# Kernel tuning notes

Measured on AMD Instinct MI355X. Metric: run time of the kernel, lower is better.

## Reference

```python
import jax, jax.numpy as jnp
import numpy as np

D_MODEL = 1024
N_HEADS = 16
D_K = D_MODEL // N_HEADS
B, S = 4, 2048
NEG = -1e9


def setup_inputs() -> dict:
    key = jax.random.key(0)
    ks = jax.random.split(key, 9)
    scale = 1.0 / np.sqrt(D_MODEL)
    x = jax.random.normal(ks[0], (B, S, D_MODEL), dtype=jnp.float32)
    mask = jnp.tril(jnp.ones((S, S), dtype=jnp.int32))  # causal lower-triangular
    Wq = jax.random.normal(ks[1], (D_MODEL, D_MODEL), dtype=jnp.float32) * scale
    Wk = jax.random.normal(ks[2], (D_MODEL, D_MODEL), dtype=jnp.float32) * scale
    Wv = jax.random.normal(ks[3], (D_MODEL, D_MODEL), dtype=jnp.float32) * scale
    Wo = jax.random.normal(ks[4], (D_MODEL, D_MODEL), dtype=jnp.float32) * scale
    bq = jnp.zeros((D_MODEL,), dtype=jnp.float32)
    bk = jnp.zeros((D_MODEL,), dtype=jnp.float32)
    bv = jnp.zeros((D_MODEL,), dtype=jnp.float32)
    bo = jnp.zeros((D_MODEL,), dtype=jnp.float32)
    return {"x": x, "mask": mask, "Wq": Wq, "bq": bq, "Wk": Wk, "bk": bk,
            "Wv": Wv, "bv": bv, "Wo": Wo, "bo": bo}


def reference(x, mask, Wq, bq, Wk, bk, Wv, bv, Wo, bo):
    b, s, _ = x.shape
    # nn.Linear: y = x @ W.T + b
    Q = x @ Wq.T + bq
    K = x @ Wk.T + bk
    V = x @ Wv.T + bv
    # [b, h, s, d_k]
    Q = Q.reshape(b, s, N_HEADS, D_K).transpose(0, 2, 1, 3)
    K = K.reshape(b, s, N_HEADS, D_K).transpose(0, 2, 1, 3)
    V = V.reshape(b, s, N_HEADS, D_K).transpose(0, 2, 1, 3)
    score = jnp.einsum('bhqd,bhkd->bhqk', Q, K) / jnp.sqrt(jnp.float32(D_K))
    score = jnp.where(mask == 0, jnp.float32(NEG), score)
    attn = jax.nn.softmax(score, axis=-1)
    out = jnp.einsum('bhqk,bhkd->bhqd', attn, V)
    out = out.transpose(0, 2, 1, 3).reshape(b, s, D_MODEL)
    return out @ Wo.T + bo
```

## Files before the change

### kernel.cpp

```cpp
#include <hip/hip_runtime.h>
#include <hip/hip_bf16.h>
#include <stdint.h>

typedef __bf16 bf16x8 __attribute__((ext_vector_type(8)));
typedef float  f32x4  __attribute__((ext_vector_type(4)));

#define B_   4
#define S_   2048
#define DM   1024
#define H_   16
#define DK   64
#define M_TOT 8192

__device__ __forceinline__ void gld16(const __bf16* g, char* l) {
    __builtin_amdgcn_global_load_lds(
        (const __attribute__((address_space(1))) void*)g,
        (__attribute__((address_space(3))) void*)l,
        16, 0, 0);
}

__global__ __launch_bounds__(256)
void cvt_f32_bf16(const float* __restrict__ in, __bf16* __restrict__ out, int n) {
    int i = (blockIdx.x * 256 + threadIdx.x) * 8;
    if (i >= n) return;
    float4 a = *(const float4*)(in + i);
    float4 c = *(const float4*)(in + i + 4);
    bf16x8 o;
    o[0] = (__bf16)a.x; o[1] = (__bf16)a.y; o[2] = (__bf16)a.z; o[3] = (__bf16)a.w;
    o[4] = (__bf16)c.x; o[5] = (__bf16)c.y; o[6] = (__bf16)c.z; o[7] = (__bf16)c.w;
    *(bf16x8*)(out + i) = o;
}

__global__ __launch_bounds__(256)
void cvt4_w(const float* __restrict__ w0, const float* __restrict__ w1,
            const float* __restrict__ w2, const float* __restrict__ w3,
            __bf16* __restrict__ out) {
    const int z = blockIdx.z;
    const float* in = (z == 0) ? w0 : (z == 1) ? w1 : (z == 2) ? w2 : w3;
    int i = (blockIdx.x * 256 + threadIdx.x) * 8;
    float4 a = *(const float4*)(in + i);
    float4 c = *(const float4*)(in + i + 4);
    bf16x8 o;
    o[0] = (__bf16)a.x; o[1] = (__bf16)a.y; o[2] = (__bf16)a.z; o[3] = (__bf16)a.w;
    o[4] = (__bf16)c.x; o[5] = (__bf16)c.y; o[6] = (__bf16)c.z; o[7] = (__bf16)c.w;
    *(bf16x8*)(out + (size_t)z * (DM * DM) + i) = o;
}

__device__ __forceinline__ void gemm_core(const __bf16* __restrict__ A,
                                          const __bf16* __restrict__ W,
                                          int m0, int n0,
                                          f32x4 (&acc)[4][4]) {
    __shared__ __bf16 As[128 * 32];
    __shared__ __bf16 Bs[128 * 32];
    const int tid  = threadIdx.x;
    const int wid  = tid >> 6;
    const int lane = tid & 63;
    const int ln15 = lane & 15, lg = lane >> 4;
    const int wr = (wid >> 1) * 64;
    const int wc = (wid & 1) * 64;

    const int c1 = tid, c2 = tid + 256;
    const int ar1 = m0 + (c1 >> 2), ac1 = (c1 & 3) * 8;
    const int ar2 = m0 + (c2 >> 2), ac2 = (c2 & 3) * 8;
    const int br1 = n0 + (c1 >> 2);
    const int br2 = n0 + (c2 >> 2);
    char* la1 = (char*)As + wid * 1024;
    char* la2 = la1 + 4096;
    char* lb1 = (char*)Bs + wid * 1024;
    char* lb2 = lb1 + 4096;

    for (int k0 = 0; k0 < DM; k0 += 32) {
        gld16(A + (size_t)ar1 * DM + k0 + ac1, la1);
        gld16(A + (size_t)ar2 * DM + k0 + ac2, la2);
        gld16(W + (size_t)br1 * DM + k0 + ac1, lb1);
        gld16(W + (size_t)br2 * DM + k0 + ac2, lb2);
        __syncthreads();
        bf16x8 af[4], bfr[4];
#pragma unroll
        for (int m = 0; m < 4; ++m)
            af[m] = *(const bf16x8*)&As[(wr + m * 16 + ln15) * 32 + lg * 8];
#pragma unroll
        for (int n = 0; n < 4; ++n)
            bfr[n] = *(const bf16x8*)&Bs[(wc + n * 16 + ln15) * 32 + lg * 8];
#pragma unroll
        for (int m = 0; m < 4; ++m)
#pragma unroll
            for (int n = 0; n < 4; ++n)
                acc[m][n] = __builtin_amdgcn_mfma_f32_16x16x32_bf16(af[m], bfr[n], acc[m][n], 0, 0, 0);
        __syncthreads();
    }
}

__global__ __launch_bounds__(256)
void gemm_qkv_kernel(const __bf16* __restrict__ Xb,
                     const __bf16* __restrict__ Wq, const __bf16* __restrict__ Wk,
                     const __bf16* __restrict__ Wv,
                     const float* __restrict__ bq, const float* __restrict__ bk,
                     const float* __restrict__ bv,
                     __bf16* __restrict__ Qb, __bf16* __restrict__ Kb,
                     __bf16* __restrict__ Vt) {
    const int z = blockIdx.z;
    const __bf16* W   = (z == 0) ? Wq : (z == 1) ? Wk : Wv;
    const float* bias = (z == 0) ? bq : (z == 1) ? bk : bv;
    const int m0 = blockIdx.x * 128, n0 = blockIdx.y * 128;

    f32x4 acc[4][4] = {};
    gemm_core(Xb, W, m0, n0, acc);

    const int tid = threadIdx.x, wid = tid >> 6, lane = tid & 63;
    const int ln15 = lane & 15, lg = lane >> 4;
    const int wr = (wid >> 1) * 64, wc = (wid & 1) * 64;
    const float oscl = (z == 0) ? 0.18033688f : 1.0f;

    if (z < 2) {
        __bf16* out = (z == 0) ? Qb : Kb;
#pragma unroll
        for (int ni = 0; ni < 4; ++ni) {
            int col = n0 + wc + ni * 16 + ln15;
            int h = col >> 6, d = col & 63;
            float bval = bias[col];
#pragma unroll
            for (int mi = 0; mi < 4; ++mi)
#pragma unroll
                for (int r = 0; r < 4; ++r) {
                    int row = m0 + wr + mi * 16 + lg * 4 + r;
                    int b = row >> 11, s = row & 2047;
                    out[(((size_t)(b * H_ + h)) * S_ + s) * DK + d] =
                        (__bf16)((acc[mi][ni][r] + bval) * oscl);
                }
        }
    } else {
#pragma unroll
        for (int ni = 0; ni < 4; ++ni) {
            int col = n0 + wc + ni * 16 + ln15;
            int h = col >> 6, d = col & 63;
            float bval = bias[col];
#pragma unroll
            for (int mi = 0; mi < 4; ++mi)
#pragma unroll
                for (int r = 0; r < 4; ++r) {
                    int row = m0 + wr + mi * 16 + lg * 4 + r;
                    int b = row >> 11, s = row & 2047;
                    Vt[(((size_t)(b * H_ + h)) * DK + d) * S_ + s] =
                        (__bf16)(acc[mi][ni][r] + bval);
                }
        }
    }
}

__global__ __launch_bounds__(256)
void gemm_out_kernel(const __bf16* __restrict__ Ab, const __bf16* __restrict__ Wo,
                     const float* __restrict__ bo, float* __restrict__ out) {
    const int m0 = blockIdx.x * 128, n0 = blockIdx.y * 128;
    f32x4 acc[4][4] = {};
    gemm_core(Ab, Wo, m0, n0, acc);

    const int tid = threadIdx.x, wid = tid >> 6, lane = tid & 63;
    const int ln15 = lane & 15, lg = lane >> 4;
    const int wr = (wid >> 1) * 64, wc = (wid & 1) * 64;
#pragma unroll
    for (int ni = 0; ni < 4; ++ni) {
        int col = n0 + wc + ni * 16 + ln15;
        float bval = bo[col];
#pragma unroll
        for (int mi = 0; mi < 4; ++mi)
#pragma unroll
            for (int r = 0; r < 4; ++r) {
                int row = m0 + wr + mi * 16 + lg * 4 + r;
                out[(size_t)row * DM + col] = acc[mi][ni][r] + bval;
            }
    }
}

__global__ __launch_bounds__(512)
void attn_kernel(const __bf16* __restrict__ Qb, const __bf16* __restrict__ Kb,
                 const __bf16* __restrict__ Vt, __bf16* __restrict__ AO) {
    __shared__ __bf16 Ks[2][64 * 64];
    __shared__ __bf16 Vs[2][64 * 64];

    const int tid = threadIdx.x, wid = tid >> 6, lane = tid & 63;
    const int ln15 = lane & 15, lg = lane >> 4;
    const int bh = blockIdx.y;
    const size_t base = (size_t)bh * (S_ * DK);
    const int b = bh >> 4, h = bh & 15;

    const int sr = tid >> 3;
    const int sc = ((tid & 7) ^ (sr & 7)) * 8;
    const int swz = (ln15 & 7) << 3;

    const __bf16* kgb = Kb + base;
    const __bf16* vgb = Vt + base;

    auto stage = [&](int buf, int kt) {
        char* dk = (char*)Ks + buf * 8192 + wid * 1024;
        char* dv = (char*)Vs + buf * 8192 + wid * 1024;
        gld16(kgb + (size_t)(kt * 64 + sr) * DK + sc, dk);
        gld16(vgb + (size_t)sr * S_ + kt * 64 + sc, dv);
    };

#pragma unroll
    for (int ph = 0; ph < 2; ++ph) {
        const int qb   = ph ? (int)blockIdx.x : 15 - (int)blockIdx.x;
        const int last = 2 * qb + 1;
        const int dt   = 2 * qb + (wid >> 2);
        const int qr0  = qb * 128 + wid * 16 + ln15;

        bf16x8 qf[2];
        {
            int q0 = qb * 128 + wid * 16 + ln15;
            qf[0] = *(const bf16x8*)&Qb[base + (size_t)q0 * DK + lg * 8];
            qf[1] = *(const bf16x8*)&Qb[base + (size_t)q0 * DK + 32 + lg * 8];
        }

        f32x4 acc[4] = {};
        float m0 = -1e30f;
        float l0p = 0.f;

        stage(0, 0);
        asm volatile("s_waitcnt vmcnt(0)" ::: "memory");
        __builtin_amdgcn_s_barrier();
        __builtin_amdgcn_sched_barrier(0);

        for (int kt = 0; kt <= last; ++kt) {
            const int cur = kt & 1;
            if (kt < last) stage(cur ^ 1, kt + 1);

            const __bf16* ksb = &Ks[cur][0];
            const __bf16* vsb = &Vs[cur][0];

            f32x4 z[4] = {};
            __builtin_amdgcn_s_setprio(1);
#pragma unroll
            for (int cb = 0; cb < 4; ++cb)
#pragma unroll
                for (int kk = 0; kk < 2; ++kk) {
                    bf16x8 kf = *(const bf16x8*)&ksb[(cb * 16 + ln15) * 64 + ((kk * 32 + lg * 8) ^ swz)];
                    z[cb] = __builtin_amdgcn_mfma_f32_16x16x32_bf16(kf, qf[kk], z[cb], 0, 0, 0);
                }
            __builtin_amdgcn_s_setprio(0);

            if (kt >= dt) {
                const int kcb = kt * 64 + lg * 4;
#pragma unroll
                for (int cb = 0; cb < 4; ++cb)
#pragma unroll
                    for (int r = 0; r < 4; ++r)
                        if (kcb + cb * 16 + r > qr0) z[cb][r] = -3e8f;
            }

            float lx0;
            {
                f32x4 a = z[0], bb = z[1];
#pragma unroll
                for (int r = 0; r < 4; ++r) { a[r] = fmaxf(a[r], z[2][r]); bb[r] = fmaxf(bb[r], z[3][r]); }
                lx0 = fmaxf(fmaxf(fmaxf(a[0], a[1]), fmaxf(a[2], a[3])),
                            fmaxf(fmaxf(bb[0], bb[1]), fmaxf(bb[2], bb[3])));
            }
            if (__any(lx0 > m0 + 8.f)) {
                float pm0 = lx0;
                pm0 = fmaxf(pm0, __shfl_xor(pm0, 16)); pm0 = fmaxf(pm0, __shfl_xor(pm0, 32));
                float mn0 = fmaxf(m0, pm0), sv0 = exp2f(m0 - mn0); m0 = mn0; l0p *= sv0;
#pragma unroll
                for (int r = 0; r < 4; ++r) {
                    float b0 = __shfl(sv0, lg * 4 + r);
#pragma unroll
                    for (int db = 0; db < 4; ++db) acc[db][r] *= b0;
                }
            }

            float ts0 = 0.f;
            uint32_t a0[4], b0[4];
#pragma unroll
            for (int cb = 0; cb < 4; ++cb) {
                float e0 = exp2f(z[cb][0] - m0), e1 = exp2f(z[cb][1] - m0);
                float e2 = exp2f(z[cb][2] - m0), e3 = exp2f(z[cb][3] - m0);
                ts0 += (e0 + e1) + (e2 + e3);
                asm("v_cvt_pk_bf16_f32 %0, %1, %2" : "=v"(a0[cb]) : "v"(e0), "v"(e1));
                asm("v_cvt_pk_bf16_f32 %0, %1, %2" : "=v"(b0[cb]) : "v"(e2), "v"(e3));
            }
            l0p += ts0;

            union U8 { uint32_t u[4]; bf16x8 v; };
            bf16x8 pa[2];
#pragma unroll
            for (int kk = 0; kk < 2; ++kk) {
                uint32_t x = a0[2 * kk], y = a0[2 * kk + 1];
                asm("v_permlane32_swap_b32 %0, %1" : "+v"(x), "+v"(y));
                asm("v_permlane16_swap_b32 %0, %1" : "+v"(x), "+v"(y));
                uint32_t p = b0[2 * kk], q = b0[2 * kk + 1];
                asm("v_permlane32_swap_b32 %0, %1" : "+v"(p), "+v"(q));
                asm("v_permlane16_swap_b32 %0, %1" : "+v"(p), "+v"(q));
                U8 f; f.u[0] = x; f.u[1] = p; f.u[2] = y; f.u[3] = q;
                pa[kk] = f.v;
            }

            __builtin_amdgcn_s_setprio(1);
#pragma unroll
            for (int db = 0; db < 4; ++db)
#pragma unroll
                for (int kk = 0; kk < 2; ++kk) {
                    bf16x8 vf = *(const bf16x8*)&vsb[(db * 16 + ln15) * 64 + ((kk * 32 + lg * 8) ^ swz)];
                    acc[db] = __builtin_amdgcn_mfma_f32_16x16x32_bf16(pa[kk], vf, acc[db], 0, 0, 0);
                }
            __builtin_amdgcn_s_setprio(0);

            if (kt < last) {
                asm volatile("s_waitcnt vmcnt(0)" ::: "memory");
                __builtin_amdgcn_s_barrier();
                __builtin_amdgcn_sched_barrier(0);
            }
        }

        float l0 = l0p;
        l0 += __shfl_xor(l0, 16); l0 += __shfl_xor(l0, 32);
        float i0 = 1.f / l0;
#pragma unroll
        for (int r = 0; r < 4; ++r) {
            float b0 = __shfl(i0, lg * 4 + r);
            int s0r = qb * 128 + wid * 16 + lg * 4 + r;
#pragma unroll
            for (int db = 0; db < 4; ++db)
                AO[((size_t)(b * S_ + s0r)) * DM + h * DK + db * 16 + ln15] = (__bf16)(acc[db][r] * b0);
        }
    }
}

extern "C" void kernel_launch(void* const* d_in, const int* in_sizes, int n_in,
                              void* d_out, int out_size, void* d_ws, size_t ws_size,
                              hipStream_t stream) {
    const float* x  = (const float*)d_in[0];
    const float* Wq = (const float*)d_in[2];
    const float* bq = (const float*)d_in[3];
    const float* Wk = (const float*)d_in[4];
    const float* bk = (const float*)d_in[5];
    const float* Wv = (const float*)d_in[6];
    const float* bv = (const float*)d_in[7];
    const float* Wo = (const float*)d_in[8];
    const float* bo = (const float*)d_in[9];
    float* out = (float*)d_out;

    char* ws = (char*)d_ws;
    __bf16* xb  = (__bf16*)ws;
    __bf16* wqb = (__bf16*)(ws + 16777216);
    __bf16* wkb = wqb + 1048576;
    __bf16* wvb = wkb + 1048576;
    __bf16* wob = wvb + 1048576;
    __bf16* Qb  = (__bf16*)(ws + 25165824);
    __bf16* Kb  = Qb + 8388608;
    __bf16* Vt  = Kb + 8388608;
    __bf16* AO  = xb;

    cvt_f32_bf16<<<4096, 256, 0, stream>>>(x, xb, M_TOT * DM);
    cvt4_w<<<dim3(512, 1, 4), 256, 0, stream>>>(Wq, Wk, Wv, Wo, wqb);

    gemm_qkv_kernel<<<dim3(64, 8, 3), 256, 0, stream>>>(xb, wqb, wkb, wvb,
                                                        bq, bk, bv, Qb, Kb, Vt);
    attn_kernel<<<dim3(8, 64), 512, 0, stream>>>(Qb, Kb, Vt, AO);
    gemm_out_kernel<<<dim3(64, 8), 256, 0, stream>>>(AO, wob, bo, out);
}
```

Measured before the change: 193.9 us.

## Widen attention KV tile to 128 and compute row sums via MFMA with ones

Doubles the K/V tile per iteration from 64 to 128 keys, halving the number of barrier-synchronized loop iterations and staging rounds, with the causal mask applied only on the final tile. The softmax denominator is now accumulated by an extra MFMA of the probability fragment against a vector of ones, replacing the per-lane scalar sums and cross-lane shuffles. This costs double the LDS footprint and more registers for the wider score tile. Waves whose rows lie in the first half of the diagonal tile now also compute the fully masked upper half.

```diff
diff --git a/kernel.cpp b/kernel.cpp
--- a/kernel.cpp
+++ b/kernel.cpp
@@ -175,8 +175,8 @@
 __global__ __launch_bounds__(512)
 void attn_kernel(const __bf16* __restrict__ Qb, const __bf16* __restrict__ Kb,
                  const __bf16* __restrict__ Vt, __bf16* __restrict__ AO) {
-    __shared__ __bf16 Ks[2][64 * 64];
-    __shared__ __bf16 Vs[2][64 * 64];
+    __shared__ __bf16 Ks[2][128 * 64];
+    __shared__ __bf16 Vs[2][64 * 128];
 
     const int tid = threadIdx.x, wid = tid >> 6, lane = tid & 63;
     const int ln15 = lane & 15, lg = lane >> 4;
@@ -184,38 +184,46 @@
     const size_t base = (size_t)bh * (S_ * DK);
     const int b = bh >> 4, h = bh & 15;
 
-    const int sr = tid >> 3;
-    const int sc = ((tid & 7) ^ (sr & 7)) * 8;
-    const int swz = (ln15 & 7) << 3;
+    const int krow = wid * 8 + (lane >> 3);
+    const int kswz = ((lane & 7) ^ (krow & 7)) * 8;
+    const int vrow = wid * 4 + (lane >> 4);
+    const int vswz = ((lane & 15) ^ (vrow & 7)) * 8;
+    const int swz  = (ln15 & 7) << 3;
 
     const __bf16* kgb = Kb + base;
     const __bf16* vgb = Vt + base;
 
     auto stage = [&](int buf, int kt) {
-        char* dk = (char*)Ks + buf * 8192 + wid * 1024;
-        char* dv = (char*)Vs + buf * 8192 + wid * 1024;
-        gld16(kgb + (size_t)(kt * 64 + sr) * DK + sc, dk);
-        gld16(vgb + (size_t)sr * S_ + kt * 64 + sc, dv);
+        char* dk = (char*)Ks + buf * 16384 + wid * 1024;
+        char* dv = (char*)Vs + buf * 16384 + wid * 1024;
+        gld16(kgb + (size_t)(kt * 128 + krow) * DK + kswz, dk);
+        gld16(kgb + (size_t)(kt * 128 + krow + 64) * DK + kswz, dk + 8192);
+        gld16(vgb + (size_t)vrow * S_ + kt * 128 + vswz, dv);
+        gld16(vgb + (size_t)(vrow + 32) * S_ + kt * 128 + vswz, dv + 8192);
     };
+
+    bf16x8 ones;
+#pragma unroll
+    for (int j = 0; j < 8; ++j) ones[j] = (__bf16)1.0f;
 
 #pragma unroll
     for (int ph = 0; ph < 2; ++ph) {
         const int qb   = ph ? (int)blockIdx.x : 15 - (int)blockIdx.x;
-        const int last = 2 * qb + 1;
-        const int dt   = 2 * qb + (wid >> 2);
+        const int last = qb;
         const int qr0  = qb * 128 + wid * 16 + ln15;
 
         bf16x8 qf[2];
         {
-            int q0 = qb * 128 + wid * 16 + ln15;
+            int q0 = qr0;
             qf[0] = *(const bf16x8*)&Qb[base + (size_t)q0 * DK + lg * 8];
             qf[1] = *(const bf16x8*)&Qb[base + (size_t)q0 * DK + 32 + lg * 8];
         }
 
         f32x4 acc[4] = {};
+        f32x4 lacc = {};
         float m0 = -1e30f;
-        float l0p = 0.f;
-
+
+        __builtin_amdgcn_s_barrier();
         stage(0, 0);
         asm volatile("s_waitcnt vmcnt(0)" ::: "memory");
         __builtin_amdgcn_s_barrier();
@@ -228,10 +236,10 @@
             const __bf16* ksb = &Ks[cur][0];
             const __bf16* vsb = &Vs[cur][0];
 
-            f32x4 z[4] = {};
+            f32x4 z[8] = {};
             __builtin_amdgcn_s_setprio(1);
 #pragma unroll
-            for (int cb = 0; cb < 4; ++cb)
+            for (int cb = 0; cb < 8; ++cb)
 #pragma unroll
                 for (int kk = 0; kk < 2; ++kk) {
                     bf16x8 kf = *(const bf16x8*)&ksb[(cb * 16 + ln15) * 64 + ((kk * 32 + lg * 8) ^ swz)];
@@ -239,10 +247,10 @@
                 }
             __builtin_amdgcn_s_setprio(0);
 
-            if (kt >= dt) {
-                const int kcb = kt * 64 + lg * 4;
-#pragma unroll
-                for (int cb = 0; cb < 4; ++cb)
+            if (kt == last) {
+                const int kcb = kt * 128 + lg * 4;
+#pragma unroll
+                for (int cb = 0; cb < 8; ++cb)
 #pragma unroll
                     for (int r = 0; r < 4; ++r)
                         if (kcb + cb * 16 + r > qr0) z[cb][r] = -3e8f;
@@ -250,58 +258,59 @@
 
             float lx0;
             {
-                f32x4 a = z[0], bb = z[1];
-#pragma unroll
-                for (int r = 0; r < 4; ++r) { a[r] = fmaxf(a[r], z[2][r]); bb[r] = fmaxf(bb[r], z[3][r]); }
-                lx0 = fmaxf(fmaxf(fmaxf(a[0], a[1]), fmaxf(a[2], a[3])),
-                            fmaxf(fmaxf(bb[0], bb[1]), fmaxf(bb[2], bb[3])));
+                f32x4 a = z[0];
+#pragma unroll
+                for (int cb = 1; cb < 8; ++cb)
+#pragma unroll
+                    for (int r = 0; r < 4; ++r) a[r] = fmaxf(a[r], z[cb][r]);
+                lx0 = fmaxf(fmaxf(fmaxf(a[0], a[1]), a[2]), a[3]);
             }
             if (__any(lx0 > m0 + 8.f)) {
                 float pm0 = lx0;
                 pm0 = fmaxf(pm0, __shfl_xor(pm0, 16)); pm0 = fmaxf(pm0, __shfl_xor(pm0, 32));
-                float mn0 = fmaxf(m0, pm0), sv0 = exp2f(m0 - mn0); m0 = mn0; l0p *= sv0;
+                float mn0 = fmaxf(m0, pm0), sv0 = exp2f(m0 - mn0); m0 = mn0;
 #pragma unroll
                 for (int r = 0; r < 4; ++r) {
                     float b0 = __shfl(sv0, lg * 4 + r);
+                    lacc[r] *= b0;
 #pragma unroll
                     for (int db = 0; db < 4; ++db) acc[db][r] *= b0;
                 }
             }
 
-            float ts0 = 0.f;
-            uint32_t a0[4], b0[4];
-#pragma unroll
-            for (int cb = 0; cb < 4; ++cb) {
+            uint32_t a0[8], b0[8];
+#pragma unroll
+            for (int cb = 0; cb < 8; ++cb) {
                 float e0 = exp2f(z[cb][0] - m0), e1 = exp2f(z[cb][1] - m0);
                 float e2 = exp2f(z[cb][2] - m0), e3 = exp2f(z[cb][3] - m0);
-                ts0 += (e0 + e1) + (e2 + e3);
                 asm("v_cvt_pk_bf16_f32 %0, %1, %2" : "=v"(a0[cb]) : "v"(e0), "v"(e1));
                 asm("v_cvt_pk_bf16_f32 %0, %1, %2" : "=v"(b0[cb]) : "v"(e2), "v"(e3));
             }
-            l0p += ts0;
 
             union U8 { uint32_t u[4]; bf16x8 v; };
-            bf16x8 pa[2];
-#pragma unroll
-            for (int kk = 0; kk < 2; ++kk) {
-                uint32_t x = a0[2 * kk], y = a0[2 * kk + 1];
+            bf16x8 pa[4];
+#pragma unroll
+            for (int ks = 0; ks < 4; ++ks) {
+                uint32_t x = a0[2 * ks], y = a0[2 * ks + 1];
                 asm("v_permlane32_swap_b32 %0, %1" : "+v"(x), "+v"(y));
                 asm("v_permlane16_swap_b32 %0, %1" : "+v"(x), "+v"(y));
-                uint32_t p = b0[2 * kk], q = b0[2 * kk + 1];
+                uint32_t p = b0[2 * ks], q = b0[2 * ks + 1];
                 asm("v_permlane32_swap_b32 %0, %1" : "+v"(p), "+v"(q));
                 asm("v_permlane16_swap_b32 %0, %1" : "+v"(p), "+v"(q));
                 U8 f; f.u[0] = x; f.u[1] = p; f.u[2] = y; f.u[3] = q;
-                pa[kk] = f.v;
+                pa[ks] = f.v;
             }
 
             __builtin_amdgcn_s_setprio(1);
 #pragma unroll
-            for (int db = 0; db < 4; ++db)
-#pragma unroll
-                for (int kk = 0; kk < 2; ++kk) {
-                    bf16x8 vf = *(const bf16x8*)&vsb[(db * 16 + ln15) * 64 + ((kk * 32 + lg * 8) ^ swz)];
-                    acc[db] = __builtin_amdgcn_mfma_f32_16x16x32_bf16(pa[kk], vf, acc[db], 0, 0, 0);
-                }
+            for (int ks = 0; ks < 4; ++ks) {
+                lacc = __builtin_amdgcn_mfma_f32_16x16x32_bf16(pa[ks], ones, lacc, 0, 0, 0);
+#pragma unroll
+                for (int db = 0; db < 4; ++db) {
+                    bf16x8 vf = *(const bf16x8*)&vsb[(db * 16 + ln15) * 128 + ((ks * 32 + lg * 8) ^ swz)];
+                    acc[db] = __builtin_amdgcn_mfma_f32_16x16x32_bf16(pa[ks], vf, acc[db], 0, 0, 0);
+                }
+            }
             __builtin_amdgcn_s_setprio(0);
 
             if (kt < last) {
@@ -311,16 +320,13 @@
             }
         }
 
-        float l0 = l0p;
-        l0 += __shfl_xor(l0, 16); l0 += __shfl_xor(l0, 32);
-        float i0 = 1.f / l0;
 #pragma unroll
         for (int r = 0; r < 4; ++r) {
-            float b0 = __shfl(i0, lg * 4 + r);
+            float i0 = 1.f / lacc[r];
             int s0r = qb * 128 + wid * 16 + lg * 4 + r;
 #pragma unroll
             for (int db = 0; db < 4; ++db)
-                AO[((size_t)(b * S_ + s0r)) * DM + h * DK + db * 16 + ln15] = (__bf16)(acc[db][r] * b0);
+                AO[((size_t)(b * S_ + s0r)) * DM + h * DK + db * 16 + ln15] = (__bf16)(acc[db][r] * i0);
         }
     }
 }
```

Result: faster. 189.8 us (-2.1%).
